# Performance work log

Hardware: AMD Instinct MI355X
Metric: run time of the kernel (lower is better)

## Reference

```python
import jax, jax.numpy as jnp
import numpy as np

N = 20000
E = 320000
HEADS = 4
CH = [128, 256, 256]


def setup_inputs() -> dict:
    key = jax.random.key(0)
    ks = jax.random.split(key, 16)
    x = jax.random.normal(ks[0], (N, CH[0]), dtype=jnp.float32)
    edge_index = jax.random.randint(ks[1], (2, E), 0, N, dtype=jnp.int64)

    def glorot(k, shape, fan_in):
        return jax.random.normal(k, shape, dtype=jnp.float32) / np.float32(np.sqrt(fan_in))

    # Block 0: FeaStConv 128 -> 256, skip Linear 128 -> 256
    W0 = glorot(ks[2], (CH[0], HEADS * CH[1]), CH[0])
    u0 = glorot(ks[3], (CH[0], HEADS), CH[0])
    c0 = jnp.zeros((HEADS,), jnp.float32)
    b0 = jnp.zeros((CH[1],), jnp.float32)
    skipW0 = glorot(ks[4], (CH[0], CH[1]), CH[0])
    skipb0 = jnp.zeros((CH[1],), jnp.float32)
    # Block 1: FeaStConv 256 -> 256, identity skip
    W1 = glorot(ks[5], (CH[1], HEADS * CH[2]), CH[1])
    u1 = glorot(ks[6], (CH[1], HEADS), CH[1])
    c1 = jnp.zeros((HEADS,), jnp.float32)
    b1 = jnp.zeros((CH[2],), jnp.float32)
    return {"x": x, "edge_index": edge_index,
            "W0": W0, "u0": u0, "c0": c0, "b0": b0,
            "skipW0": skipW0, "skipb0": skipb0,
            "W1": W1, "u1": u1, "c1": c1, "b1": b1}


def feast_conv(x, src, dst, W, u, c, b):
    """FeaStConv: out_i = b + mean_{j in N(i)} sum_h softmax_h(u_h.(x_j-x_i)+c_h) * W_h x_j."""
    n = x.shape[0]
    out_ch = W.shape[1] // HEADS
    y = (x @ W).reshape(n, HEADS, out_ch)              # [N, H, out]
    q = jax.nn.softmax((x[src] - x[dst]) @ u + c, -1)  # [E', H]
    msg = jnp.einsum('eh,ehd->ed', q, y[src])          # [E', out]
    s = jax.ops.segment_sum(msg, dst, num_segments=n)
    cnt = jax.ops.segment_sum(jnp.ones(src.shape, x.dtype), dst, num_segments=n)
    return s / jnp.maximum(cnt, 1.0)[:, None] + b


def reference(x, edge_index, W0, u0, c0, b0, skipW0, skipb0, W1, u1, c1, b1):
    n = x.shape[0]
    loop = jnp.arange(n, dtype=edge_index.dtype)       # self-loops (PyG default)
    src = jnp.concatenate([edge_index[0], loop])
    dst = jnp.concatenate([edge_index[1], loop])
    # ResBlock 0: relu(conv(x) + linear skip) -- channels change 128->256
    h = jax.nn.relu(feast_conv(x, src, dst, W0, u0, c0, b0) + x @ skipW0 + skipb0)
    # ResBlock 1: relu(conv(h) + identity skip)
    h = jax.nn.relu(feast_conv(h, src, dst, W1, u1, c1, b1) + h)
    return (h, edge_index)
```

## Files before the change

### kernel.cpp

```cpp
#include <hip/hip_runtime.h>
#include <hip/hip_bf16.h>

typedef __hip_bfloat16 bf16;

typedef short bf16x8 __attribute__((ext_vector_type(8)));
typedef float f32x4  __attribute__((ext_vector_type(4)));

__device__ __forceinline__ float bflo(unsigned v){ union{unsigned u; float f;} c; c.u = v << 16; return c.f; }
__device__ __forceinline__ float bfhi(unsigned v){ union{unsigned u; float f;} c; c.u = v & 0xffff0000u; return c.f; }
__device__ __forceinline__ unsigned cvtpk_bf16(float lo, float hi){
  unsigned r;
  asm("v_cvt_pk_bf16_f32 %0, %1, %2" : "=v"(r) : "v"(lo), "v"(hi));
  return r;
}

__device__ __forceinline__ void dev_t32(
    const bf16* __restrict__ B, int ldB, int sr, int sc,
    bf16* __restrict__ Bt, int ldBt, int dr, int dc,
    int t, bf16 (*tile)[33])
{
  const int tx = t & 31, ty = t >> 5;
  #pragma unroll
  for (int i = 0; i < 32; i += 8)
    tile[ty + i][tx] = B[(size_t)(sr + ty + i) * ldB + sc + tx];
  __syncthreads();
  #pragma unroll
  for (int i = 0; i < 32; i += 8)
    Bt[(size_t)(dr + ty + i) * ldBt + dc + tx] = tile[tx][ty + i];
}

__global__ __launch_bounds__(256) void prep_kernel(
    const bf16* __restrict__ x, const int* __restrict__ ei,
    const bf16* __restrict__ W0, const bf16* __restrict__ sW0,
    const bf16* __restrict__ W1, const bf16* __restrict__ u0,
    bf16* __restrict__ Btc0, bf16* __restrict__ Bt1,
    int* __restrict__ cursor, int* __restrict__ ssrc,
    float* __restrict__ eout, float4* __restrict__ p0,
    int N, int E, int b5)
{
  __shared__ bf16 tile[32][33];
  const int bid = blockIdx.x;
  const int t   = threadIdx.x;

  if (bid < 128) {
    const int bx = bid & 31, by = bid >> 5;
    dev_t32(W0, 1024, by * 32, bx * 32,
            Btc0, 640, (bx & 7) * 32, (bx >> 3) * 128 + by * 32, t, tile);
  } else if (bid < 160) {
    const int lb = bid - 128, bx = lb & 7, by = lb >> 3;
    dev_t32(sW0, 256, by * 32, bx * 32,
            Btc0, 640, bx * 32, 512 + by * 32, t, tile);
  } else if (bid < 416) {
    const int lb = bid - 160, bx = lb & 31, by = lb >> 5;
    dev_t32(W1, 1024, by * 32, bx * 32,
            Bt1, 1024, (bx & 7) * 32, (bx >> 3) * 256 + by * 32, t, tile);
  } else if (bid < b5) {
    const int i = (bid - 416) * 256 + t;
    if (i < 2 * E) {
      const int v = ei[i];
      eout[i] = (float)v;
      if (i < E) {
        const int d   = ei[E + i];
        const int pos = atomicAdd(cursor + d, 1);
        if (pos < 64) ssrc[(d << 6) + pos] = v;
      }
    }
  } else {
    const int node = (bid - b5) * 4 + (t >> 6);
    if (node >= N) return;
    const int lane = t & 63;
    const unsigned xv = ((const unsigned*)(x + (size_t)node * 128))[lane];
    const float d0 = bflo(xv), d1 = bfhi(xv);
    const uint4 uv = *(const uint4*)(u0 + (size_t)lane * 8);
    float t0 = d0 * bflo(uv.x) + d1 * bflo(uv.z);
    float t1 = d0 * bfhi(uv.x) + d1 * bfhi(uv.z);
    float t2 = d0 * bflo(uv.y) + d1 * bflo(uv.w);
    float t3 = d0 * bfhi(uv.y) + d1 * bfhi(uv.w);
    #pragma unroll
    for (int off = 32; off > 0; off >>= 1) {
      t0 += __shfl_xor(t0, off);
      t1 += __shfl_xor(t1, off);
      t2 += __shfl_xor(t2, off);
      t3 += __shfl_xor(t3, off);
    }
    if (lane == 0) p0[node] = make_float4(t0, t1, t2, t3);
  }
}

template<int MODE>
__global__ __launch_bounds__(256) void gemm_cat_kernel(
    const bf16* __restrict__ A1, int K1, const bf16* __restrict__ A2, int K2,
    const bf16* __restrict__ Bt, int ldBt, int M,
    const bf16* __restrict__ bias1, const bf16* __restrict__ bias2,
    const bf16* __restrict__ hadd, bf16* __restrict__ outb,
    float* __restrict__ outf)
{
  __shared__ __align__(16) bf16 As[64 * 64];
  __shared__ __align__(16) bf16 Bs[64 * 64];

  const int tid  = threadIdx.x;
  const int col0 = blockIdx.x * 64;
  const int row0 = blockIdx.y * 64;
  const int lane = tid & 63;
  const int wave = tid >> 6;
  const int wm   = wave & 1, wn = wave >> 1;
  const int ln   = lane & 15, quad = lane >> 4;
  const int K    = K1 + K2;

  f32x4 acc[2][2] = {};

  for (int k0 = 0; k0 < K; k0 += 64) {
    #pragma unroll
    for (int rep = 0; rep < 2; ++rep) {
      const int c  = tid + rep * 256;
      const int r  = c >> 3;
      const int kp = (c & 7) << 3;
      const int gr = min(row0 + r, M - 1);
      const int kk = k0 + kp;
      uint4 va;
      if (kk < K1) va = *(const uint4*)(A1 + (size_t)gr * K1 + kk);
      else         va = *(const uint4*)(A2 + (size_t)gr * K2 + (kk - K1));
      *(uint4*)(As + r * 64 + (kp ^ ((r & 7) << 3))) = va;
    }
    #pragma unroll
    for (int rep = 0; rep < 2; ++rep) {
      const int c  = tid + rep * 256;
      const int r  = c >> 3;
      const int kp = (c & 7) << 3;
      *(uint4*)(Bs + r * 64 + (kp ^ ((r & 7) << 3))) =
          *(const uint4*)(Bt + (size_t)(col0 + r) * ldBt + k0 + kp);
    }
    __syncthreads();

    bf16x8 a[2][2], b[2][2];
    #pragma unroll
    for (int mi = 0; mi < 2; ++mi) {
      const int rr = wm * 32 + mi * 16 + ln;
      #pragma unroll
      for (int ks = 0; ks < 2; ++ks)
        a[mi][ks] = *(const bf16x8*)(As + rr * 64 + ((ks * 32 + quad * 8) ^ ((rr & 7) << 3)));
    }
    #pragma unroll
    for (int ni = 0; ni < 2; ++ni) {
      const int rr = wn * 32 + ni * 16 + ln;
      #pragma unroll
      for (int ks = 0; ks < 2; ++ks)
        b[ni][ks] = *(const bf16x8*)(Bs + rr * 64 + ((ks * 32 + quad * 8) ^ ((rr & 7) << 3)));
    }
    #pragma unroll
    for (int ks = 0; ks < 2; ++ks)
      #pragma unroll
      for (int mi = 0; mi < 2; ++mi)
        #pragma unroll
        for (int ni = 0; ni < 2; ++ni)
          acc[mi][ni] = __builtin_amdgcn_mfma_f32_16x16x32_bf16(a[mi][ks], b[ni][ks], acc[mi][ni], 0, 0, 0);
    __syncthreads();
  }

  #pragma unroll
  for (int mi = 0; mi < 2; ++mi) {
    const int rbase = row0 + wm * 32 + mi * 16 + quad * 4;
    #pragma unroll
    for (int ni = 0; ni < 2; ++ni) {
      const int col = col0 + wn * 32 + ni * 16 + ln;
      float bb = __bfloat162float(bias1[col]);
      if (MODE == 0) bb += __bfloat162float(bias2[col]);
      #pragma unroll
      for (int r = 0; r < 4; ++r) {
        const int gr = rbase + r;
        if (gr >= M) continue;
        const size_t idx = (size_t)gr * 256 + col;
        float v = acc[mi][ni][r] + bb;
        if (MODE == 1) v += __bfloat162float(hadd[idx]);
        v = fmaxf(v, 0.f);
        if (MODE == 0) outb[idx] = __float2bfloat16(v);
        else           outf[idx] = v;
      }
    }
  }
}

__global__ __launch_bounds__(256) void proj256_kernel(
    const bf16* __restrict__ h, const bf16* __restrict__ u,
    float4* __restrict__ p, int N)
{
  const int node = (int)(((unsigned)blockIdx.x * 256u + threadIdx.x) >> 6);
  if (node >= N) return;
  const int lane = threadIdx.x & 63;
  const uint2 hv = *(const uint2*)(h + (size_t)node * 256 + lane * 4);
  const float d0 = bflo(hv.x), d1 = bfhi(hv.x);
  const float d2 = bflo(hv.y), d3 = bfhi(hv.y);
  const uint4 ua = *(const uint4*)(u + (size_t)lane * 16);
  const uint4 ub = *(const uint4*)(u + (size_t)lane * 16 + 8);
  float t0 = d0*bflo(ua.x) + d1*bflo(ua.z) + d2*bflo(ub.x) + d3*bflo(ub.z);
  float t1 = d0*bfhi(ua.x) + d1*bfhi(ua.z) + d2*bfhi(ub.x) + d3*bfhi(ub.z);
  float t2 = d0*bflo(ua.y) + d1*bflo(ua.w) + d2*bflo(ub.y) + d3*bflo(ub.w);
  float t3 = d0*bfhi(ua.y) + d1*bfhi(ua.w) + d2*bfhi(ub.y) + d3*bfhi(ub.w);
  #pragma unroll
  for (int off = 32; off > 0; off >>= 1) {
    t0 += __shfl_xor(t0, off);
    t1 += __shfl_xor(t1, off);
    t2 += __shfl_xor(t2, off);
    t3 += __shfl_xor(t3, off);
  }
  if (lane == 0) p[node] = make_float4(t0, t1, t2, t3);
}

template<int CIN>
__global__ __launch_bounds__(256) void passF_kernel(
    const int* __restrict__ cnt, const int* __restrict__ ssrc,
    const float4* __restrict__ p, const bf16* __restrict__ feat,
    const bf16* __restrict__ cvec, bf16* __restrict__ F, int N)
{
  __shared__ int    s_src[4][64];
  __shared__ float4 s_q[4][64];

  const int t = threadIdx.x;
  const int g = t >> 6;
  const int l = t & 63;
  const int i = blockIdx.x * 4 + g;
  if (i >= N) return;

  const int h2 = l >> 5;
  const int c  = l & 31;
  const int beg = i << 6;
  const int deg = min(cnt[i], 64);

  constexpr int CPL = (CIN == 128) ? 4 : 8;
  constexpr int SH  = (CIN == 128) ? 8 : 9;
  const unsigned coff = (unsigned)c * (CPL * 2);
  const char* fb = (const char*)feat;

  const float cc0 = __bfloat162float(cvec[0]), cc1 = __bfloat162float(cvec[1]);
  const float cc2 = __bfloat162float(cvec[2]), cc3 = __bfloat162float(cvec[3]);
  const float4 pd = p[i];

  float f[4][CPL];
  #pragma unroll
  for (int h = 0; h < 4; ++h)
    #pragma unroll
    for (int k = 0; k < CPL; ++k) f[h][k] = 0.f;

#define PF_ACC(OFF, QX, QY, QZ, QW)                                            \
  if constexpr (CIN == 128) {                                                  \
    const uint2 v_ = *(const uint2*)(fb + (OFF));                              \
    const float d0 = bflo(v_.x), d1 = bfhi(v_.x);                              \
    const float d2 = bflo(v_.y), d3 = bfhi(v_.y);                              \
    f[0][0] += (QX)*d0; f[0][1] += (QX)*d1; f[0][2] += (QX)*d2; f[0][3] += (QX)*d3; \
    f[1][0] += (QY)*d0; f[1][1] += (QY)*d1; f[1][2] += (QY)*d2; f[1][3] += (QY)*d3; \
    f[2][0] += (QZ)*d0; f[2][1] += (QZ)*d1; f[2][2] += (QZ)*d2; f[2][3] += (QZ)*d3; \
    f[3][0] += (QW)*d0; f[3][1] += (QW)*d1; f[3][2] += (QW)*d2; f[3][3] += (QW)*d3; \
  } else {                                                                     \
    const uint4 v_ = *(const uint4*)(fb + (OFF));                              \
    const float d0 = bflo(v_.x), d1 = bfhi(v_.x);                              \
    const float d2 = bflo(v_.y), d3 = bfhi(v_.y);                              \
    const float d4 = bflo(v_.z), d5 = bfhi(v_.z);                              \
    const float d6 = bflo(v_.w), d7 = bfhi(v_.w);                              \
    f[0][0] += (QX)*d0; f[0][1] += (QX)*d1; f[0][2] += (QX)*d2; f[0][3] += (QX)*d3; \
    f[0][4] += (QX)*d4; f[0][5] += (QX)*d5; f[0][6] += (QX)*d6; f[0][7] += (QX)*d7; \
    f[1][0] += (QY)*d0; f[1][1] += (QY)*d1; f[1][2] += (QY)*d2; f[1][3] += (QY)*d3; \
    f[1][4] += (QY)*d4; f[1][5] += (QY)*d5; f[1][6] += (QY)*d6; f[1][7] += (QY)*d7; \
    f[2][0] += (QZ)*d0; f[2][1] += (QZ)*d1; f[2][2] += (QZ)*d2; f[2][3] += (QZ)*d3; \
    f[2][4] += (QZ)*d4; f[2][5] += (QZ)*d5; f[2][6] += (QZ)*d6; f[2][7] += (QZ)*d7; \
    f[3][0] += (QW)*d0; f[3][1] += (QW)*d1; f[3][2] += (QW)*d2; f[3][3] += (QW)*d3; \
    f[3][4] += (QW)*d4; f[3][5] += (QW)*d5; f[3][6] += (QW)*d6; f[3][7] += (QW)*d7; \
  }

  {
    const float mx = fmaxf(fmaxf(cc0, cc1), fmaxf(cc2, cc3));
    const float e0 = __expf(cc0 - mx), e1 = __expf(cc1 - mx);
    const float e2 = __expf(cc2 - mx), e3 = __expf(cc3 - mx);
    const float sinv = 1.f / (e0 + e1 + e2 + e3);
    if (h2 == 0) {
      const unsigned off = ((unsigned)i << SH) + coff;
      PF_ACC(off, e0 * sinv, e1 * sinv, e2 * sinv, e3 * sinv)
    }
  }

#define PF_PAIR(P)                                                             \
  {                                                                            \
    const int e_ = ((P) << 1) + h2;                                            \
    const int    src_ = s_src[g][e_];                                          \
    const float4 q_   = s_q[g][e_];                                            \
    const unsigned off_ = ((unsigned)src_ << SH) + coff;                       \
    PF_ACC(off_, q_.x, q_.y, q_.z, q_.w)                                       \
  }

  if (deg > 0) {
    if (l < deg) {
      const int s = ssrc[beg + l];
      const float4 ps = p[s];
      const float t0 = ps.x - pd.x + cc0;
      const float t1 = ps.y - pd.y + cc1;
      const float t2 = ps.z - pd.z + cc2;
      const float t3 = ps.w - pd.w + cc3;
      const float mx = fmaxf(fmaxf(t0, t1), fmaxf(t2, t3));
      const float e0 = __expf(t0 - mx), e1 = __expf(t1 - mx);
      const float e2 = __expf(t2 - mx), e3 = __expf(t3 - mx);
      const float inv = 1.f / (e0 + e1 + e2 + e3);
      s_src[g][l] = s;
      s_q[g][l]   = make_float4(e0 * inv, e1 * inv, e2 * inv, e3 * inv);
    } else if (l == deg) {
      s_src[g][l] = 0;
      s_q[g][l]   = make_float4(0.f, 0.f, 0.f, 0.f);
    }
    const int np = (deg + 1) >> 1;
    int pj = 0;
    for (; pj + 8 <= np; pj += 8) {
      PF_PAIR(pj)     PF_PAIR(pj + 1) PF_PAIR(pj + 2) PF_PAIR(pj + 3)
      PF_PAIR(pj + 4) PF_PAIR(pj + 5) PF_PAIR(pj + 6) PF_PAIR(pj + 7)
    }
    for (; pj + 4 <= np; pj += 4) { PF_PAIR(pj) PF_PAIR(pj + 1) PF_PAIR(pj + 2) PF_PAIR(pj + 3) }
    for (; pj < np; ++pj) PF_PAIR(pj)
  }
#undef PF_PAIR
#undef PF_ACC

  const float s = 1.f / (float)(deg + 1);
  #pragma unroll
  for (int h = 0; h < 4; ++h)
    #pragma unroll
    for (int k = 0; k < CPL; ++k) {
      float v = f[h][k] * s;
      v += __shfl_xor(v, 32);
      f[h][k] = v;
    }

  if constexpr (CIN == 128) {
    char* dst = (char*)F + ((size_t)i << 10) + (unsigned)c * 8;
    if (h2 == 0) {
      uint2 p0v, p1v;
      p0v.x = cvtpk_bf16(f[0][0], f[0][1]); p0v.y = cvtpk_bf16(f[0][2], f[0][3]);
      p1v.x = cvtpk_bf16(f[1][0], f[1][1]); p1v.y = cvtpk_bf16(f[1][2], f[1][3]);
      *(uint2*)(dst)       = p0v;
      *(uint2*)(dst + 256) = p1v;
    } else {
      uint2 p2v, p3v;
      p2v.x = cvtpk_bf16(f[2][0], f[2][1]); p2v.y = cvtpk_bf16(f[2][2], f[2][3]);
      p3v.x = cvtpk_bf16(f[3][0], f[3][1]); p3v.y = cvtpk_bf16(f[3][2], f[3][3]);
      *(uint2*)(dst + 512) = p2v;
      *(uint2*)(dst + 768) = p3v;
    }
  } else {
    char* dst = (char*)F + ((size_t)i << 11) + (unsigned)c * 16;
    if (h2 == 0) {
      uint4 p0v, p1v;
      p0v.x = cvtpk_bf16(f[0][0], f[0][1]); p0v.y = cvtpk_bf16(f[0][2], f[0][3]);
      p0v.z = cvtpk_bf16(f[0][4], f[0][5]); p0v.w = cvtpk_bf16(f[0][6], f[0][7]);
      p1v.x = cvtpk_bf16(f[1][0], f[1][1]); p1v.y = cvtpk_bf16(f[1][2], f[1][3]);
      p1v.z = cvtpk_bf16(f[1][4], f[1][5]); p1v.w = cvtpk_bf16(f[1][6], f[1][7]);
      *(uint4*)(dst)        = p0v;
      *(uint4*)(dst + 512)  = p1v;
    } else {
      uint4 p2v, p3v;
      p2v.x = cvtpk_bf16(f[2][0], f[2][1]); p2v.y = cvtpk_bf16(f[2][2], f[2][3]);
      p2v.z = cvtpk_bf16(f[2][4], f[2][5]); p2v.w = cvtpk_bf16(f[2][6], f[2][7]);
      p3v.x = cvtpk_bf16(f[3][0], f[3][1]); p3v.y = cvtpk_bf16(f[3][2], f[3][3]);
      p3v.z = cvtpk_bf16(f[3][4], f[3][5]); p3v.w = cvtpk_bf16(f[3][6], f[3][7]);
      *(uint4*)(dst + 1024) = p2v;
      *(uint4*)(dst + 1536) = p3v;
    }
  }
}

extern "C" void kernel_launch(void* const* d_in, const int* in_sizes, int n_in,
                              void* d_out, int out_size, void* d_ws, size_t ws_size,
                              hipStream_t stream)
{
  const bf16* x   = (const bf16*)d_in[0];
  const int*  ei  = (const int*)d_in[1];
  const bf16* W0  = (const bf16*)d_in[2];
  const bf16* u0  = (const bf16*)d_in[3];
  const bf16* c0  = (const bf16*)d_in[4];
  const bf16* b0  = (const bf16*)d_in[5];
  const bf16* sW0 = (const bf16*)d_in[6];
  const bf16* sb0 = (const bf16*)d_in[7];
  const bf16* W1  = (const bf16*)d_in[8];
  const bf16* u1  = (const bf16*)d_in[9];
  const bf16* c1  = (const bf16*)d_in[10];
  const bf16* b1  = (const bf16*)d_in[11];

  const int N = in_sizes[0] / 128;
  const int E = in_sizes[1] / 2;

  char* ws = (char*)d_ws;
  bf16*   F      = (bf16*)ws;   ws += (size_t)N * 1024 * sizeof(bf16);
  bf16*   h0     = (bf16*)ws;   ws += (size_t)N * 256 * sizeof(bf16);
  float4* p0     = (float4*)ws; ws += (size_t)N * sizeof(float4);
  float4* p1     = (float4*)ws; ws += (size_t)N * sizeof(float4);
  int*    ssrc   = (int*)ws;    ws += (size_t)N * 64 * sizeof(int);
  int*    cursor = (int*)ws;    ws += (size_t)N * sizeof(int);
  bf16*   Btc0   = (bf16*)ws;   ws += (size_t)256 * 640 * sizeof(bf16);
  bf16*   Bt1    = (bf16*)ws;   ws += (size_t)256 * 1024 * sizeof(bf16);

  hipMemsetAsync(cursor, 0, (size_t)N * sizeof(int), stream);

  const int gTiles   = (N + 63) / 64;
  const int nwBlocks = (N + 3) / 4;

  const int b5 = 416 + (2 * E + 255) / 256;
  const int b6 = b5 + nwBlocks;

  prep_kernel<<<b6, 256, 0, stream>>>(x, ei, W0, sW0, W1, u0, Btc0, Bt1,
                                      cursor, ssrc,
                                      (float*)d_out + (size_t)N * 256, p0,
                                      N, E, b5);

  passF_kernel<128><<<nwBlocks, 256, 0, stream>>>(cursor, ssrc, p0, x, c0, F, N);
  gemm_cat_kernel<0><<<dim3(4, gTiles), 256, 0, stream>>>(
      F, 512, x, 128, Btc0, 640, N, b0, sb0, nullptr, h0, nullptr);

  proj256_kernel<<<nwBlocks, 256, 0, stream>>>(h0, u1, p1, N);
  passF_kernel<256><<<nwBlocks, 256, 0, stream>>>(cursor, ssrc, p1, h0, c1, F, N);
  gemm_cat_kernel<1><<<dim3(4, gTiles), 256, 0, stream>>>(
      F, 1024, nullptr, 0, Bt1, 1024, N, b1, nullptr, h0, nullptr, (float*)d_out);
}
```

Before: 216.9 us.

## Fuse layer-1 projection into GEMM epilogue, prefetch tiles, remap blocks per XCD

The separate proj256 kernel is removed. The first GEMM epilogue now computes the h0·u1 projection from fp32 values, reduces it across lanes and atomically adds partial sums into p1, which is zeroed by an enlarged memset. The GEMM main loop gains register double-buffering, so the next K tile's global loads overlap the MFMA work. Workgroup IDs are also remapped so consecutive tiles land on the same XCD for L2 reuse. This saves one kernel launch and a re-read of h0, at the cost of float atomics (nondeterministic summation order) and higher register pressure.

```diff
diff --git a/kernel.cpp b/kernel.cpp
--- a/kernel.cpp
+++ b/kernel.cpp
@@ -93,14 +93,24 @@
     const bf16* __restrict__ Bt, int ldBt, int M,
     const bf16* __restrict__ bias1, const bf16* __restrict__ bias2,
     const bf16* __restrict__ hadd, bf16* __restrict__ outb,
-    float* __restrict__ outf)
+    float* __restrict__ outf, const bf16* __restrict__ uproj,
+    float* __restrict__ pout)
 {
   __shared__ __align__(16) bf16 As[64 * 64];
   __shared__ __align__(16) bf16 Bs[64 * 64];
 
   const int tid  = threadIdx.x;
-  const int col0 = blockIdx.x * 64;
-  const int row0 = blockIdx.y * 64;
+
+  const int nwg = (int)(gridDim.x * gridDim.y);
+  int lin = (int)(blockIdx.y * gridDim.x + blockIdx.x);
+  {
+    const int q = nwg >> 3, r8 = nwg & 7;
+    const int xcd = lin & 7, pos = lin >> 3;
+    lin = (xcd < r8 ? xcd * (q + 1) : r8 * (q + 1) + (xcd - r8) * q) + pos;
+  }
+  const int col0 = (lin & 3) * 64;
+  const int row0 = (lin >> 2) * 64;
+
   const int lane = tid & 63;
   const int wave = tid >> 6;
   const int wm   = wave & 1, wn = wave >> 1;
@@ -108,29 +118,37 @@
   const int K    = K1 + K2;
 
   f32x4 acc[2][2] = {};
-
-  for (int k0 = 0; k0 < K; k0 += 64) {
-    #pragma unroll
-    for (int rep = 0; rep < 2; ++rep) {
-      const int c  = tid + rep * 256;
-      const int r  = c >> 3;
-      const int kp = (c & 7) << 3;
-      const int gr = min(row0 + r, M - 1);
-      const int kk = k0 + kp;
-      uint4 va;
-      if (kk < K1) va = *(const uint4*)(A1 + (size_t)gr * K1 + kk);
-      else         va = *(const uint4*)(A2 + (size_t)gr * K2 + (kk - K1));
-      *(uint4*)(As + r * 64 + (kp ^ ((r & 7) << 3))) = va;
-    }
-    #pragma unroll
-    for (int rep = 0; rep < 2; ++rep) {
-      const int c  = tid + rep * 256;
-      const int r  = c >> 3;
-      const int kp = (c & 7) << 3;
-      *(uint4*)(Bs + r * 64 + (kp ^ ((r & 7) << 3))) =
-          *(const uint4*)(Bt + (size_t)(col0 + r) * ldBt + k0 + kp);
-    }
-    __syncthreads();
+  uint4 ra[2], rb[2];
+
+#define GC_LOAD_TILE(K0)                                                       \
+  _Pragma("unroll")                                                            \
+  for (int rep = 0; rep < 2; ++rep) {                                          \
+    const int c  = tid + rep * 256;                                            \
+    const int r  = c >> 3;                                                     \
+    const int kp = (c & 7) << 3;                                               \
+    const int gr = min(row0 + r, M - 1);                                       \
+    const int kk = (K0) + kp;                                                  \
+    if (kk < K1) ra[rep] = *(const uint4*)(A1 + (size_t)gr * K1 + kk);         \
+    else         ra[rep] = *(const uint4*)(A2 + (size_t)gr * K2 + (kk - K1));  \
+    rb[rep] = *(const uint4*)(Bt + (size_t)(col0 + r) * ldBt + (K0) + kp);     \
+  }
+#define GC_WRITE_TILE()                                                        \
+  _Pragma("unroll")                                                            \
+  for (int rep = 0; rep < 2; ++rep) {                                          \
+    const int c  = tid + rep * 256;                                            \
+    const int r  = c >> 3;                                                     \
+    const int kp = (c & 7) << 3;                                               \
+    *(uint4*)(As + r * 64 + (kp ^ ((r & 7) << 3))) = ra[rep];                  \
+    *(uint4*)(Bs + r * 64 + (kp ^ ((r & 7) << 3))) = rb[rep];                  \
+  }
+
+  GC_LOAD_TILE(0)
+  GC_WRITE_TILE()
+  __syncthreads();
+
+  for (int k0 = 0;; k0 += 64) {
+    const bool more = (k0 + 64 < K);
+    if (more) GC_LOAD_TILE(k0 + 64)
 
     bf16x8 a[2][2], b[2][2];
     #pragma unroll
@@ -154,56 +172,60 @@
         #pragma unroll
         for (int ni = 0; ni < 2; ++ni)
           acc[mi][ni] = __builtin_amdgcn_mfma_f32_16x16x32_bf16(a[mi][ks], b[ni][ks], acc[mi][ni], 0, 0, 0);
+
+    if (!more) break;
     __syncthreads();
-  }
-
+    GC_WRITE_TILE()
+    __syncthreads();
+  }
+#undef GC_LOAD_TILE
+#undef GC_WRITE_TILE
+
+  float bb[2]; uint2 uv[2];
+  #pragma unroll
+  for (int ni = 0; ni < 2; ++ni) {
+    const int col = col0 + wn * 32 + ni * 16 + ln;
+    bb[ni] = __bfloat162float(bias1[col]);
+    if (MODE == 0) {
+      bb[ni] += __bfloat162float(bias2[col]);
+      uv[ni] = *(const uint2*)(uproj + (size_t)col * 4);
+    }
+  }
   #pragma unroll
   for (int mi = 0; mi < 2; ++mi) {
-    const int rbase = row0 + wm * 32 + mi * 16 + quad * 4;
-    #pragma unroll
-    for (int ni = 0; ni < 2; ++ni) {
-      const int col = col0 + wn * 32 + ni * 16 + ln;
-      float bb = __bfloat162float(bias1[col]);
-      if (MODE == 0) bb += __bfloat162float(bias2[col]);
+    #pragma unroll
+    for (int r = 0; r < 4; ++r) {
+      const int gr = row0 + wm * 32 + mi * 16 + quad * 4 + r;
+      if (gr >= M) continue;
+      float hs0 = 0.f, hs1 = 0.f, hs2 = 0.f, hs3 = 0.f;
       #pragma unroll
-      for (int r = 0; r < 4; ++r) {
-        const int gr = rbase + r;
-        if (gr >= M) continue;
+      for (int ni = 0; ni < 2; ++ni) {
+        const int col = col0 + wn * 32 + ni * 16 + ln;
         const size_t idx = (size_t)gr * 256 + col;
-        float v = acc[mi][ni][r] + bb;
+        float v = acc[mi][ni][r] + bb[ni];
         if (MODE == 1) v += __bfloat162float(hadd[idx]);
         v = fmaxf(v, 0.f);
         if (MODE == 0) outb[idx] = __float2bfloat16(v);
         else           outf[idx] = v;
+        if (MODE == 0) {
+          hs0 += v * bflo(uv[ni].x); hs1 += v * bfhi(uv[ni].x);
+          hs2 += v * bflo(uv[ni].y); hs3 += v * bfhi(uv[ni].y);
+        }
       }
-    }
-  }
-}
-
-__global__ __launch_bounds__(256) void proj256_kernel(
-    const bf16* __restrict__ h, const bf16* __restrict__ u,
-    float4* __restrict__ p, int N)
-{
-  const int node = (int)(((unsigned)blockIdx.x * 256u + threadIdx.x) >> 6);
-  if (node >= N) return;
-  const int lane = threadIdx.x & 63;
-  const uint2 hv = *(const uint2*)(h + (size_t)node * 256 + lane * 4);
-  const float d0 = bflo(hv.x), d1 = bfhi(hv.x);
-  const float d2 = bflo(hv.y), d3 = bfhi(hv.y);
-  const uint4 ua = *(const uint4*)(u + (size_t)lane * 16);
-  const uint4 ub = *(const uint4*)(u + (size_t)lane * 16 + 8);
-  float t0 = d0*bflo(ua.x) + d1*bflo(ua.z) + d2*bflo(ub.x) + d3*bflo(ub.z);
-  float t1 = d0*bfhi(ua.x) + d1*bfhi(ua.z) + d2*bfhi(ub.x) + d3*bfhi(ub.z);
-  float t2 = d0*bflo(ua.y) + d1*bflo(ua.w) + d2*bflo(ub.y) + d3*bflo(ub.w);
-  float t3 = d0*bfhi(ua.y) + d1*bfhi(ua.w) + d2*bfhi(ub.y) + d3*bfhi(ub.w);
-  #pragma unroll
-  for (int off = 32; off > 0; off >>= 1) {
-    t0 += __shfl_xor(t0, off);
-    t1 += __shfl_xor(t1, off);
-    t2 += __shfl_xor(t2, off);
-    t3 += __shfl_xor(t3, off);
-  }
-  if (lane == 0) p[node] = make_float4(t0, t1, t2, t3);
+      if (MODE == 0) {
+        #pragma unroll
+        for (int off = 1; off < 16; off <<= 1) {
+          hs0 += __shfl_xor(hs0, off); hs1 += __shfl_xor(hs1, off);
+          hs2 += __shfl_xor(hs2, off); hs3 += __shfl_xor(hs3, off);
+        }
+        if (ln == 0) {
+          float* pp = pout + (size_t)gr * 4;
+          atomicAdd(pp + 0, hs0); atomicAdd(pp + 1, hs1);
+          atomicAdd(pp + 2, hs2); atomicAdd(pp + 3, hs3);
+        }
+      }
+    }
+  }
 }
 
 template<int CIN>
@@ -387,13 +409,13 @@
   bf16*   F      = (bf16*)ws;   ws += (size_t)N * 1024 * sizeof(bf16);
   bf16*   h0     = (bf16*)ws;   ws += (size_t)N * 256 * sizeof(bf16);
   float4* p0     = (float4*)ws; ws += (size_t)N * sizeof(float4);
-  float4* p1     = (float4*)ws; ws += (size_t)N * sizeof(float4);
   int*    ssrc   = (int*)ws;    ws += (size_t)N * 64 * sizeof(int);
   int*    cursor = (int*)ws;    ws += (size_t)N * sizeof(int);
+  float4* p1     = (float4*)ws; ws += (size_t)N * sizeof(float4);
   bf16*   Btc0   = (bf16*)ws;   ws += (size_t)256 * 640 * sizeof(bf16);
   bf16*   Bt1    = (bf16*)ws;   ws += (size_t)256 * 1024 * sizeof(bf16);
 
-  hipMemsetAsync(cursor, 0, (size_t)N * sizeof(int), stream);
+  hipMemsetAsync(cursor, 0, (size_t)N * (sizeof(int) + sizeof(float4)), stream);
 
   const int gTiles   = (N + 63) / 64;
   const int nwBlocks = (N + 3) / 4;
@@ -408,10 +430,11 @@
 
   passF_kernel<128><<<nwBlocks, 256, 0, stream>>>(cursor, ssrc, p0, x, c0, F, N);
   gemm_cat_kernel<0><<<dim3(4, gTiles), 256, 0, stream>>>(
-      F, 512, x, 128, Btc0, 640, N, b0, sb0, nullptr, h0, nullptr);
-
-  proj256_kernel<<<nwBlocks, 256, 0, stream>>>(h0, u1, p1, N);
+      F, 512, x, 128, Btc0, 640, N, b0, sb0, nullptr, h0, nullptr,
+      u1, (float*)p1);
+
   passF_kernel<256><<<nwBlocks, 256, 0, stream>>>(cursor, ssrc, p1, h0, c1, F, N);
   gemm_cat_kernel<1><<<dim3(4, gTiles), 256, 0, stream>>>(
-      F, 1024, nullptr, 0, Bt1, 1024, N, b1, nullptr, h0, nullptr, (float*)d_out);
-}
+      F, 1024, nullptr, 0, Bt1, 1024, N, b1, nullptr, h0, nullptr, (float*)d_out,
+      nullptr, nullptr);
+}
```

Result: slower. 337.0 us (+55.4%).
